# Kernel optimization log

Hardware: AMD Instinct MI355X
Metric: run time of the kernel (lower is better)

The kernel has to match this reference:

```python
import jax, jax.numpy as jnp
import numpy as np


def setup_inputs() -> dict:
    key = jax.random.key(0)
    k1, k2, k3, k4, k5 = jax.random.split(key, 5)
    B, S, E, H, D = 8, 1024, 1024, 8, 128  # batch, seq, embed, heads, hidden/head
    stdv = 1.0 / np.sqrt(D)
    return {
        "k": jax.random.normal(k1, (B, S, E), jnp.float32),
        "q": jax.random.normal(k2, (B, S, E), jnp.float32),
        "flag": 0,  # False: project q through w_qx
        "w_kx": jax.random.uniform(k3, (H, E, D), jnp.float32, -stdv, stdv),
        "w_qx": jax.random.uniform(k4, (H, E, D), jnp.float32, -stdv, stdv),
        "proj_w": jax.random.normal(k5, (E, H * D), jnp.float32) * 0.02,  # out_dim = embed_dim
        "proj_b": jnp.zeros((E,), jnp.float32),
    }


def reference(k, q, flag, w_kx, w_qx, proj_w, proj_b):
    H, E, D = w_kx.shape
    B, Sk, _ = k.shape
    Sq = q.shape[1]
    # per-head tanh projections: [H, B, S, D]
    kx = jnp.tanh(jnp.einsum("bse,hed->hbsd", k, w_kx))
    if flag:
        qx = jnp.broadcast_to(q[None], (H,) + q.shape)  # q already in hidden space
    else:
        qx = jnp.tanh(jnp.einsum("bse,hed->hbsd", q, w_qx))
    # scaled dot product scores [H, B, Sq, Sk]
    score = jnp.einsum("hbqd,hbkd->hbqk", qx, kx) / jnp.sqrt(jnp.float32(D))
    attn = jax.nn.softmax(score, axis=-1)
    out = jnp.einsum("hbqk,hbkd->hbqd", attn, kx)  # [H, B, Sq, D]
    # concat heads: [B, Sq, H*D], then output projection (dropout p=0 is identity)
    out = jnp.transpose(out, (1, 2, 0, 3)).reshape(B, Sq, H * D)
    return out @ proj_w.T + proj_b
```

## Files before the change

### kernel.cpp

```cpp
#include <hip/hip_runtime.h>

typedef unsigned short u16;
typedef unsigned int u32;
typedef __bf16 bf16x8 __attribute__((ext_vector_type(8)));
typedef float f32x4 __attribute__((ext_vector_type(4)));

#define MFMA16(a, b, c) __builtin_amdgcn_mfma_f32_16x16x32_bf16(a, b, c, 0, 0, 0)
#define EXP2(x) __builtin_amdgcn_exp2f(x)

typedef const void __attribute__((address_space(1)))* gas1_t;
typedef void __attribute__((address_space(3)))* las3_t;

__device__ __forceinline__ void gload16(const void* g, void* l) {
  __builtin_amdgcn_global_load_lds((gas1_t)g, (las3_t)l, 16, 0, 0);
}

__device__ __forceinline__ u16 f2bf(float f) {
  union { float f; u32 u; } v; v.f = f;
  u32 r = v.u + 0x7FFFu + ((v.u >> 16) & 1u);
  return (u16)(r >> 16);
}

__device__ __forceinline__ float fast_tanh(float x) {
  float xc = fminf(fmaxf(x, -20.f), 20.f);
  float t = EXP2(xc * 2.885390081777927f);
  return (t - 1.0f) * __builtin_amdgcn_rcpf(t + 1.0f);
}

__global__ __launch_bounds__(256) void cvt_kernel(const float* __restrict__ in,
                                                  u16* __restrict__ out, int n8) {
  int i = blockIdx.x * blockDim.x + threadIdx.x;
  int stride = gridDim.x * blockDim.x;
  for (; i < n8; i += stride) {
    const float4* p = (const float4*)(in + (size_t)i * 8);
    float4 a = p[0], b = p[1];
    u16 t[8];
    t[0] = f2bf(a.x); t[1] = f2bf(a.y); t[2] = f2bf(a.z); t[3] = f2bf(a.w);
    t[4] = f2bf(b.x); t[5] = f2bf(b.y); t[6] = f2bf(b.z); t[7] = f2bf(b.w);
    *(uint4*)(out + (size_t)i * 8) = *(uint4*)t;
  }
}

__global__ __launch_bounds__(256) void wtrans_kernel(const float* __restrict__ w,
                                                     u16* __restrict__ wT) {
  __shared__ float t[64][65];
  int h = blockIdx.z;
  int e0 = blockIdx.x * 64, d0 = blockIdx.y * 64;
  const float* src = w + (size_t)h * 1024 * 128;
  u16* dst = wT + (size_t)h * 128 * 1024;
  int tid = threadIdx.x;
  {
    int row = tid >> 2, c0 = (tid & 3) * 16;
#pragma unroll
    for (int i = 0; i < 4; ++i) {
      float4 v = *(const float4*)(src + (size_t)(e0 + row) * 128 + d0 + c0 + i * 4);
      t[row][c0 + i * 4 + 0] = v.x;
      t[row][c0 + i * 4 + 1] = v.y;
      t[row][c0 + i * 4 + 2] = v.z;
      t[row][c0 + i * 4 + 3] = v.w;
    }
  }
  __syncthreads();
  {
    int dl = tid >> 2, c0 = (tid & 3) * 16;
    u16 tmp[16];
#pragma unroll
    for (int i = 0; i < 16; ++i) tmp[i] = f2bf(t[c0 + i][dl]);
    u16* o = dst + (size_t)(d0 + dl) * 1024 + e0 + c0;
    *(uint4*)o = *(uint4*)tmp;
    *(uint4*)(o + 8) = *(uint4*)(tmp + 8);
  }
}


template <int BM>
__device__ __forceinline__ void gemm8_core(const u16* __restrict__ Ab,
                                           const u16* __restrict__ Bb,
                                           int K, u16* lds,
                                           f32x4 (&acc)[BM / 32][4]) {
  constexpr int MH = BM / 64;
  constexpr int HR = BM / 4;
  constexpr int AH = (BM / 2) * 64;
  constexpr int BH = 128 * 64;
  constexpr int BUF = 2 * AH + 2 * BH;
  constexpr int LA = BM / 128;
  const int tid = threadIdx.x, lane = tid & 63, wid = tid >> 6;
  const int wr = wid >> 2, wc = wid & 3, l15 = lane & 15, g = lane >> 4;
  const int nkt = K >> 6;
  const int arow = wr * HR;
  const int brow = wc * 32;

  auto stageA = [&](u16* dstHalf, int mh, int kt) {
#pragma unroll
    for (int i = 0; i < LA; ++i) {
      int c = (wid * LA + i) * 64 + lane;
      int rr = c >> 3, src = (c & 7) ^ (rr & 7);
      int grow = (rr / HR) * (2 * HR) + mh * HR + (rr % HR);
      gload16((const char*)Ab + ((size_t)grow * K + kt * 64 + src * 8) * 2,
              (char*)dstHalf + c * 16);
    }
  };
  auto stageB = [&](u16* dstHalf, int nh, int kt) {
#pragma unroll
    for (int i = 0; i < 2; ++i) {
      int c = (wid * 2 + i) * 64 + lane;
      int cc = c >> 3, src = (c & 7) ^ (cc & 7);
      int gcol = (cc >> 5) * 64 + nh * 32 + (cc & 31);
      gload16((const char*)Bb + ((size_t)gcol * K + kt * 64 + src * 8) * 2,
              (char*)dstHalf + c * 16);
    }
  };

#define LDAF(half)                                                              \
  _Pragma("unroll") for (int m = 0; m < MH; ++m)                                \
  _Pragma("unroll") for (int kc = 0; kc < 2; ++kc) {                            \
    int r_ = arow + m * 16 + l15;                                               \
    af[m][kc] = *(const bf16x8*)((half) + r_ * 64 + (((kc * 4 + g) ^ (r_ & 7)) << 3)); \
  }
#define LDBF(half)                                                              \
  _Pragma("unroll") for (int n = 0; n < 2; ++n)                                 \
  _Pragma("unroll") for (int kc = 0; kc < 2; ++kc) {                            \
    int r_ = brow + n * 16 + l15;                                               \
    bb[n][kc] = *(const bf16x8*)((half) + r_ * 64 + (((kc * 4 + g) ^ (r_ & 7)) << 3)); \
  }
#define MFMAQ(MB, NB)                                                           \
  __builtin_amdgcn_s_setprio(1);                                                \
  _Pragma("unroll") for (int m = 0; m < MH; ++m)                                \
  _Pragma("unroll") for (int n = 0; n < 2; ++n)                                 \
  _Pragma("unroll") for (int kc = 0; kc < 2; ++kc)                              \
    acc[(MB) * MH + m][(NB) * 2 + n] =                                          \
        MFMA16(af[m][kc], bb[n][kc], acc[(MB) * MH + m][(NB) * 2 + n]);         \
  __builtin_amdgcn_s_setprio(0);

  stageA(lds, 0, 0);
  stageB(lds + 2 * AH, 0, 0);
  stageA(lds + AH, 1, 0);
  stageB(lds + 2 * AH + BH, 1, 0);
  if constexpr (BM == 256) asm volatile("s_waitcnt vmcnt(4)" ::: "memory");
  else                     asm volatile("s_waitcnt vmcnt(3)" ::: "memory");
  __builtin_amdgcn_s_barrier();

  bf16x8 af[MH][2], bb[2][2];
  for (int t = 0; t < nkt; ++t) {
    const int cur = t & 1;
    u16* A0c = lds + cur * BUF;
    u16* A1c = A0c + AH;
    u16* B0c = A0c + 2 * AH;
    u16* B1c = B0c + BH;
    u16* A0n = lds + (cur ^ 1) * BUF;
    u16* A1n = A0n + AH;
    u16* B0n = A0n + 2 * AH;
    u16* B1n = B0n + BH;
    const bool pf = (t + 1 < nkt);
    const int k1 = t + 1;

    asm volatile("s_waitcnt vmcnt(2)" ::: "memory");
    LDAF(A0c);
    LDBF(B0c);
    if (pf) stageA(A0n, 0, k1);
    __builtin_amdgcn_s_barrier();
    MFMAQ(0, 0);
    __builtin_amdgcn_s_barrier();

    if (pf) {
      if constexpr (BM == 256) asm volatile("s_waitcnt vmcnt(2)" ::: "memory");
      else                     asm volatile("s_waitcnt vmcnt(1)" ::: "memory");
    } else {
      asm volatile("s_waitcnt vmcnt(0)" ::: "memory");
    }
    LDAF(A1c);
    if (pf) stageB(B0n, 0, k1);
    __builtin_amdgcn_s_barrier();
    MFMAQ(1, 0);
    __builtin_amdgcn_s_barrier();

    LDBF(B1c);
    if (pf) stageA(A1n, 1, k1);
    __builtin_amdgcn_s_barrier();
    MFMAQ(1, 1);
    __builtin_amdgcn_s_barrier();

    if (pf) {
      if constexpr (BM == 256) asm volatile("s_waitcnt vmcnt(2)" ::: "memory");
      else                     asm volatile("s_waitcnt vmcnt(1)" ::: "memory");
    }
    LDAF(A0c);
    if (pf) stageB(B1n, 1, k1);
    __builtin_amdgcn_s_barrier();
    MFMAQ(0, 1);
    __builtin_amdgcn_s_barrier();
  }
#undef LDAF
#undef LDBF
#undef MFMAQ
}

__global__ __launch_bounds__(512, 2) void gemm_tanh_kernel(
    const u16* __restrict__ Ak, const u16* __restrict__ Aq,
    const u16* __restrict__ wTk, const u16* __restrict__ wTq,
    u16* __restrict__ kxo, u16* __restrict__ qxo) {
  __shared__ alignas(16) u16 lds[2 * (2 * 128 * 64 + 2 * 128 * 64)];
  const u16* A; const u16* W; u16* C;
  if (blockIdx.z == 0) { A = Ak; W = wTk; C = kxo; }
  else { A = Aq; W = wTq; C = qxo; }
  int mBase = blockIdx.x * 256;
  int nBase = blockIdx.y * 256;
  f32x4 acc[8][4];
#pragma unroll
  for (int i = 0; i < 8; ++i)
#pragma unroll
    for (int j = 0; j < 4; ++j) acc[i][j] = (f32x4){0.f, 0.f, 0.f, 0.f};
  gemm8_core<256>(A + (size_t)mBase * 1024, W + (size_t)nBase * 1024, 1024,
                  lds, acc);
  const int lane = threadIdx.x & 63, wid = threadIdx.x >> 6;
  const int wr = wid >> 2, wc = wid & 3, l15 = lane & 15, g = lane >> 4;
#pragma unroll
  for (int mf = 0; mf < 8; ++mf)
#pragma unroll
    for (int nf = 0; nf < 4; ++nf)
#pragma unroll
      for (int j = 0; j < 4; ++j) {
        int m = mBase + wr * 128 + mf * 16 + g * 4 + j;
        int n = nBase + wc * 64 + nf * 16 + l15;
        int h = n >> 7, d = n & 127;
        C[(size_t)h * 8192 * 128 + (size_t)m * 128 + d] =
            f2bf(fast_tanh(acc[mf][nf][j]));
      }
}

__global__ __launch_bounds__(256) void transpose_kernel(const u16* __restrict__ kx,
                                                        u16* __restrict__ kxT) {
  __shared__ u16 t[64][72];
  int hb = blockIdx.z;
  const u16* src = kx + (size_t)hb * 1024 * 128;
  u16* dst = kxT + (size_t)hb * 128 * 1024;
  int s0 = blockIdx.x * 64, d0 = blockIdx.y * 64;
  int tid = threadIdx.x;
#pragma unroll
  for (int r = 0; r < 2; ++r) {
    int row = r * 32 + (tid >> 3), c8 = (tid & 7) * 8;
    uint4 v = *(const uint4*)(src + (size_t)(s0 + row) * 128 + d0 + c8);
    *(uint4*)&t[row][c8] = v;
  }
  __syncthreads();
#pragma unroll
  for (int r = 0; r < 2; ++r) {
    int dl = r * 32 + (tid >> 3), s8 = (tid & 7) * 8;
    u16 tmp[8];
#pragma unroll
    for (int i = 0; i < 8; ++i) tmp[i] = t[s8 + i][dl];
    *(uint4*)(dst + (size_t)(d0 + dl) * 1024 + s0 + s8) = *(uint4*)tmp;
  }
}

__global__ __launch_bounds__(256, 2) void attn_kernel(const u16* __restrict__ qx,
                                                      const u16* __restrict__ kx,
                                                      const u16* __restrict__ kxT,
                                                      u16* __restrict__ X) {
  __shared__ alignas(16) u16 Klds[2][64 * 128];
  __shared__ alignas(16) u16 Vlds[2][128 * 64];
  __shared__ alignas(16) u16 Plds[4][32 * 64];
  const int tid = threadIdx.x, lane = tid & 63, wid = tid >> 6;
  const int g = lane >> 4;
  const int hb = blockIdx.x, qt = blockIdx.y, h = hb >> 3, b = hb & 7;
  const u16* qxh = qx + ((size_t)h * 8192 + (size_t)b * 1024) * 128;
  const u16* kxh = kx + ((size_t)h * 8192 + (size_t)b * 1024) * 128;
  const u16* kxTh = kxT + (size_t)hb * 128 * 1024;
  const int q0 = qt * 128 + wid * 32;
  const float SC = 0.08838834764831845f * 1.44269504088896340f;

#define STAGE(buf, kt_)                                                        \
  do {                                                                         \
    _Pragma("unroll") for (int i_ = 0; i_ < 4; ++i_) {                         \
      int cIdx = (wid * 4 + i_) * 64 + lane;                                   \
      {                                                                        \
        int row = cIdx >> 4, slot = cIdx & 15;                                 \
        int src = slot ^ (row & 7);                                            \
        gload16((const char*)kxh + (size_t)((kt_) * 64 + row) * 256 + src * 16,\
                (char*)&Klds[buf][0] + (wid * 4 + i_) * 1024);                 \
      }                                                                        \
      {                                                                        \
        int row = cIdx >> 3, slot = cIdx & 7;                                  \
        int src = slot ^ (row & 7);                                            \
        gload16((const char*)kxTh + (size_t)row * 2048 + (kt_) * 128 + src * 16,\
                (char*)&Vlds[buf][0] + (wid * 4 + i_) * 1024);                 \
      }                                                                        \
    }                                                                          \
  } while (0)

  bf16x8 qa[2][4];
#pragma unroll
  for (int m = 0; m < 2; ++m)
#pragma unroll
    for (int kc = 0; kc < 4; ++kc)
      qa[m][kc] = *(const bf16x8*)(qxh + (size_t)(q0 + m * 16 + (lane & 15)) * 128
                                   + kc * 32 + g * 8);

  f32x4 os[2][8];
#pragma unroll
  for (int i = 0; i < 2; ++i)
#pragma unroll
    for (int j = 0; j < 8; ++j) os[i][j] = (f32x4){0.f, 0.f, 0.f, 0.f};
  float lsum[2] = {0.f, 0.f};

  u16* Pw = &Plds[wid][0];

  STAGE(0, 0);

  for (int kt = 0; kt < 16; ++kt) {
    const int cur = kt & 1;
    if (kt < 15) {
      STAGE(cur ^ 1, kt + 1);
      asm volatile("s_waitcnt vmcnt(8)" ::: "memory");
    } else {
      asm volatile("s_waitcnt vmcnt(0)" ::: "memory");
    }
    __builtin_amdgcn_s_barrier();

    const u16* Kc = &Klds[cur][0];
    const u16* Vc = &Vlds[cur][0];

    f32x4 sa[4][2];
#pragma unroll
    for (int i = 0; i < 4; ++i)
#pragma unroll
      for (int j = 0; j < 2; ++j) sa[i][j] = (f32x4){0.f, 0.f, 0.f, 0.f};
    __builtin_amdgcn_s_setprio(1);
#pragma unroll
    for (int kc = 0; kc < 4; ++kc) {
      bf16x8 kb[4];
#pragma unroll
      for (int t = 0; t < 4; ++t) {
        int row = t * 16 + (lane & 15);
        int ch = kc * 4 + g;
        kb[t] = *(const bf16x8*)(Kc + row * 128 + ((ch ^ (row & 7)) << 3));
      }
#pragma unroll
      for (int t = 0; t < 4; ++t)
#pragma unroll
        for (int m = 0; m < 2; ++m)
          sa[t][m] = MFMA16(kb[t], qa[m][kc], sa[t][m]);
    }
    __builtin_amdgcn_s_setprio(0);

#pragma unroll
    for (int m = 0; m < 2; ++m) {
      int q = m * 16 + (lane & 15);
      int rowb = q * 128, q7 = q & 7;
#pragma unroll
      for (int t = 0; t < 4; ++t) {
        float p0 = EXP2(sa[t][m][0] * SC);
        float p1 = EXP2(sa[t][m][1] * SC);
        float p2 = EXP2(sa[t][m][2] * SC);
        float p3 = EXP2(sa[t][m][3] * SC);
        lsum[m] += (p0 + p1) + (p2 + p3);
        uint2 pk;
        pk.x = (u32)f2bf(p0) | ((u32)f2bf(p1) << 16);
        pk.y = (u32)f2bf(p2) | ((u32)f2bf(p3) << 16);
        int slot = (2 * t + (g >> 1)) ^ q7;
        *(uint2*)((char*)Pw + rowb + slot * 16 + 8 * (g & 1)) = pk;
      }
    }

    __builtin_amdgcn_s_setprio(1);
#pragma unroll
    for (int kc2 = 0; kc2 < 2; ++kc2) {
      bf16x8 pa[2], vb[8];
#pragma unroll
      for (int m = 0; m < 2; ++m) {
        int q = m * 16 + (lane & 15);
        int slot = (g + 4 * kc2) ^ (q & 7);
        pa[m] = *(const bf16x8*)((char*)Pw + q * 128 + slot * 16);
      }
#pragma unroll
      for (int nd = 0; nd < 8; ++nd) {
        int row = nd * 16 + (lane & 15);
        int ch = kc2 * 4 + g;
        vb[nd] = *(const bf16x8*)(Vc + row * 64 + ((ch ^ (row & 7)) << 3));
      }
#pragma unroll
      for (int m = 0; m < 2; ++m)
#pragma unroll
        for (int nd = 0; nd < 8; ++nd)
          os[m][nd] = MFMA16(pa[m], vb[nd], os[m][nd]);
    }
    __builtin_amdgcn_s_setprio(0);
    __builtin_amdgcn_s_barrier();
  }
#undef STAGE

#pragma unroll
  for (int m = 0; m < 2; ++m) {
    float s = lsum[m];
    s += __shfl_xor(s, 16);
    s += __shfl_xor(s, 32);
    lsum[m] = s;
  }

#pragma unroll
  for (int m = 0; m < 2; ++m)
#pragma unroll
    for (int j = 0; j < 4; ++j) {
      float tot = __shfl(lsum[m], 4 * g + j, 64);
      float inv = 1.f / tot;
      int qrow = b * 1024 + q0 + m * 16 + g * 4 + j;
#pragma unroll
      for (int nd = 0; nd < 8; ++nd) {
        int col = h * 128 + nd * 16 + (lane & 15);
        X[(size_t)qrow * 1024 + col] = f2bf(os[m][nd][j] * inv);
      }
    }
}

__global__ __launch_bounds__(512, 2) void gemm_bias_kernel(
    const u16* __restrict__ X, const u16* __restrict__ pw,
    const float* __restrict__ pb, float* __restrict__ out) {
  __shared__ alignas(16) u16 lds[2 * (2 * 64 * 64 + 2 * 128 * 64)];
  int mBase = blockIdx.x * 128;
  int nBase = blockIdx.y * 256;
  f32x4 acc[4][4];
#pragma unroll
  for (int i = 0; i < 4; ++i)
#pragma unroll
    for (int j = 0; j < 4; ++j) acc[i][j] = (f32x4){0.f, 0.f, 0.f, 0.f};
  gemm8_core<128>(X + (size_t)mBase * 1024, pw + (size_t)nBase * 1024, 1024,
                  lds, acc);
  const int lane = threadIdx.x & 63, wid = threadIdx.x >> 6;
  const int wr = wid >> 2, wc = wid & 3, l15 = lane & 15, g = lane >> 4;
#pragma unroll
  for (int nf = 0; nf < 4; ++nf) {
    int e = nBase + wc * 64 + nf * 16 + l15;
    float bv = pb[e];
#pragma unroll
    for (int mf = 0; mf < 4; ++mf)
#pragma unroll
      for (int j = 0; j < 4; ++j) {
        int m = mBase + wr * 64 + mf * 16 + g * 4 + j;
        out[(size_t)m * 1024 + e] = acc[mf][nf][j] + bv;
      }
  }
}

extern "C" void kernel_launch(void* const* d_in, const int* in_sizes, int n_in,
                              void* d_out, int out_size, void* d_ws, size_t ws_size,
                              hipStream_t stream) {
  const float* k = (const float*)d_in[0];
  const float* q = (const float*)d_in[1];
  const float* wk = (const float*)d_in[3];
  const float* wq = (const float*)d_in[4];
  const float* pw = (const float*)d_in[5];
  const float* pb = (const float*)d_in[6];
  float* out = (float*)d_out;
  char* ws = (char*)d_ws;

  u16* kbf = (u16*)(ws);
  u16* qbf = (u16*)(ws + (16ull << 20));
  u16* wTk = (u16*)(ws + (32ull << 20));
  u16* wTq = (u16*)(ws + (34ull << 20));
  u16* pwb = (u16*)(ws + (36ull << 20));
  u16* kx  = (u16*)(ws + (38ull << 20));
  u16* qx  = (u16*)(ws + (54ull << 20));
  u16* kxT = (u16*)(ws + (70ull << 20));
  u16* X   = kbf;

  cvt_kernel<<<2048, 256, 0, stream>>>(k, kbf, 1048576);
  cvt_kernel<<<2048, 256, 0, stream>>>(q, qbf, 1048576);
  cvt_kernel<<<512, 256, 0, stream>>>(pw, pwb, 131072);
  wtrans_kernel<<<dim3(16, 2, 8), 256, 0, stream>>>(wk, wTk);
  wtrans_kernel<<<dim3(16, 2, 8), 256, 0, stream>>>(wq, wTq);
  gemm_tanh_kernel<<<dim3(32, 4, 2), 512, 0, stream>>>(kbf, qbf, wTk, wTq, kx, qx);
  transpose_kernel<<<dim3(16, 2, 64), 256, 0, stream>>>(kx, kxT);
  attn_kernel<<<dim3(64, 8), 256, 0, stream>>>(qx, kx, kxT, X);
  gemm_bias_kernel<<<dim3(64, 4), 512, 0, stream>>>(X, pwb, pb, out);
}
```

Before: 137.5 us.

## Fuse kx transpose into projection GEMM, widen attention blocks, reorder grid

The projection GEMM epilogue now also writes the transposed K tile, which removes the separate transpose kernel launch and its extra read and write of kx. The attention kernel now runs 512 threads per block, covering 256 queries per block with 8 waves, so each staged K/V tile is shared across more query rows. Each wave issues fewer loads per stage, and the wait count is adjusted to match. The grid axes for both GEMMs are swapped so consecutive blocks share the same A rows, and the LDS destination for the global-to-LDS loads is rewritten as a per-wave base. Risks are uncoalesced 8-byte strided stores for kxT in the epilogue and lower attention occupancy at the larger block size.

```diff
diff --git a/kernel.cpp b/kernel.cpp
--- a/kernel.cpp
+++ b/kernel.cpp
@@ -71,7 +71,6 @@
     *(uint4*)(o + 8) = *(uint4*)(tmp + 8);
   }
 }
-
 
 template <int BM>
 __device__ __forceinline__ void gemm8_core(const u16* __restrict__ Ab,
@@ -97,7 +96,7 @@
       int rr = c >> 3, src = (c & 7) ^ (rr & 7);
       int grow = (rr / HR) * (2 * HR) + mh * HR + (rr % HR);
       gload16((const char*)Ab + ((size_t)grow * K + kt * 64 + src * 8) * 2,
-              (char*)dstHalf + c * 16);
+              (char*)dstHalf + (wid * LA + i) * 1024);
     }
   };
   auto stageB = [&](u16* dstHalf, int nh, int kt) {
@@ -107,7 +106,7 @@
       int cc = c >> 3, src = (c & 7) ^ (cc & 7);
       int gcol = (cc >> 5) * 64 + nh * 32 + (cc & 31);
       gload16((const char*)Bb + ((size_t)gcol * K + kt * 64 + src * 8) * 2,
-              (char*)dstHalf + c * 16);
+              (char*)dstHalf + (wid * 2 + i) * 1024);
     }
   };
 
@@ -198,13 +197,14 @@
 __global__ __launch_bounds__(512, 2) void gemm_tanh_kernel(
     const u16* __restrict__ Ak, const u16* __restrict__ Aq,
     const u16* __restrict__ wTk, const u16* __restrict__ wTq,
-    u16* __restrict__ kxo, u16* __restrict__ qxo) {
+    u16* __restrict__ kxo, u16* __restrict__ qxo, u16* __restrict__ kxT) {
   __shared__ alignas(16) u16 lds[2 * (2 * 128 * 64 + 2 * 128 * 64)];
   const u16* A; const u16* W; u16* C;
   if (blockIdx.z == 0) { A = Ak; W = wTk; C = kxo; }
   else { A = Aq; W = wTq; C = qxo; }
-  int mBase = blockIdx.x * 256;
-  int nBase = blockIdx.y * 256;
+  const bool isK = (blockIdx.z == 0);
+  int nBase = blockIdx.x * 256;
+  int mBase = blockIdx.y * 256;
   f32x4 acc[8][4];
 #pragma unroll
   for (int i = 0; i < 8; ++i)
@@ -217,73 +217,55 @@
 #pragma unroll
   for (int mf = 0; mf < 8; ++mf)
 #pragma unroll
-    for (int nf = 0; nf < 4; ++nf)
+    for (int nf = 0; nf < 4; ++nf) {
+      int m0 = mBase + wr * 128 + mf * 16 + g * 4;
+      int n = nBase + wc * 64 + nf * 16 + l15;
+      int h = n >> 7, d = n & 127;
+      u16 t4[4];
 #pragma unroll
       for (int j = 0; j < 4; ++j) {
-        int m = mBase + wr * 128 + mf * 16 + g * 4 + j;
-        int n = nBase + wc * 64 + nf * 16 + l15;
-        int h = n >> 7, d = n & 127;
-        C[(size_t)h * 8192 * 128 + (size_t)m * 128 + d] =
-            f2bf(fast_tanh(acc[mf][nf][j]));
-      }
-}
-
-__global__ __launch_bounds__(256) void transpose_kernel(const u16* __restrict__ kx,
-                                                        u16* __restrict__ kxT) {
-  __shared__ u16 t[64][72];
-  int hb = blockIdx.z;
-  const u16* src = kx + (size_t)hb * 1024 * 128;
-  u16* dst = kxT + (size_t)hb * 128 * 1024;
-  int s0 = blockIdx.x * 64, d0 = blockIdx.y * 64;
-  int tid = threadIdx.x;
-#pragma unroll
-  for (int r = 0; r < 2; ++r) {
-    int row = r * 32 + (tid >> 3), c8 = (tid & 7) * 8;
-    uint4 v = *(const uint4*)(src + (size_t)(s0 + row) * 128 + d0 + c8);
-    *(uint4*)&t[row][c8] = v;
-  }
-  __syncthreads();
-#pragma unroll
-  for (int r = 0; r < 2; ++r) {
-    int dl = r * 32 + (tid >> 3), s8 = (tid & 7) * 8;
-    u16 tmp[8];
-#pragma unroll
-    for (int i = 0; i < 8; ++i) tmp[i] = t[s8 + i][dl];
-    *(uint4*)(dst + (size_t)(d0 + dl) * 1024 + s0 + s8) = *(uint4*)tmp;
-  }
-}
-
-__global__ __launch_bounds__(256, 2) void attn_kernel(const u16* __restrict__ qx,
+        t4[j] = f2bf(fast_tanh(acc[mf][nf][j]));
+        C[(size_t)h * 8192 * 128 + (size_t)(m0 + j) * 128 + d] = t4[j];
+      }
+      if (isK) {
+        int b = m0 >> 10, s0 = m0 & 1023;
+        *(uint2*)(kxT + (size_t)(h * 8 + b) * 131072 + (size_t)d * 1024 + s0) =
+            *(uint2*)t4;
+      }
+    }
+}
+
+__global__ __launch_bounds__(512, 2) void attn_kernel(const u16* __restrict__ qx,
                                                       const u16* __restrict__ kx,
                                                       const u16* __restrict__ kxT,
                                                       u16* __restrict__ X) {
   __shared__ alignas(16) u16 Klds[2][64 * 128];
   __shared__ alignas(16) u16 Vlds[2][128 * 64];
-  __shared__ alignas(16) u16 Plds[4][32 * 64];
+  __shared__ alignas(16) u16 Plds[8][32 * 64];
   const int tid = threadIdx.x, lane = tid & 63, wid = tid >> 6;
   const int g = lane >> 4;
   const int hb = blockIdx.x, qt = blockIdx.y, h = hb >> 3, b = hb & 7;
   const u16* qxh = qx + ((size_t)h * 8192 + (size_t)b * 1024) * 128;
   const u16* kxh = kx + ((size_t)h * 8192 + (size_t)b * 1024) * 128;
   const u16* kxTh = kxT + (size_t)hb * 128 * 1024;
-  const int q0 = qt * 128 + wid * 32;
+  const int q0 = qt * 256 + wid * 32;
   const float SC = 0.08838834764831845f * 1.44269504088896340f;
 
 #define STAGE(buf, kt_)                                                        \
   do {                                                                         \
-    _Pragma("unroll") for (int i_ = 0; i_ < 4; ++i_) {                         \
-      int cIdx = (wid * 4 + i_) * 64 + lane;                                   \
+    _Pragma("unroll") for (int i_ = 0; i_ < 2; ++i_) {                         \
+      int cIdx = (wid * 2 + i_) * 64 + lane;                                   \
       {                                                                        \
         int row = cIdx >> 4, slot = cIdx & 15;                                 \
         int src = slot ^ (row & 7);                                            \
         gload16((const char*)kxh + (size_t)((kt_) * 64 + row) * 256 + src * 16,\
-                (char*)&Klds[buf][0] + (wid * 4 + i_) * 1024);                 \
+                (char*)&Klds[buf][0] + (wid * 2 + i_) * 1024);                 \
       }                                                                        \
       {                                                                        \
         int row = cIdx >> 3, slot = cIdx & 7;                                  \
         int src = slot ^ (row & 7);                                            \
         gload16((const char*)kxTh + (size_t)row * 2048 + (kt_) * 128 + src * 16,\
-                (char*)&Vlds[buf][0] + (wid * 4 + i_) * 1024);                 \
+                (char*)&Vlds[buf][0] + (wid * 2 + i_) * 1024);                 \
       }                                                                        \
     }                                                                          \
   } while (0)
@@ -311,7 +293,7 @@
     const int cur = kt & 1;
     if (kt < 15) {
       STAGE(cur ^ 1, kt + 1);
-      asm volatile("s_waitcnt vmcnt(8)" ::: "memory");
+      asm volatile("s_waitcnt vmcnt(4)" ::: "memory");
     } else {
       asm volatile("s_waitcnt vmcnt(0)" ::: "memory");
     }
@@ -416,8 +398,8 @@
     const u16* __restrict__ X, const u16* __restrict__ pw,
     const float* __restrict__ pb, float* __restrict__ out) {
   __shared__ alignas(16) u16 lds[2 * (2 * 64 * 64 + 2 * 128 * 64)];
-  int mBase = blockIdx.x * 128;
-  int nBase = blockIdx.y * 256;
+  int nBase = blockIdx.x * 256;
+  int mBase = blockIdx.y * 128;
   f32x4 acc[4][4];
 #pragma unroll
   for (int i = 0; i < 4; ++i)
@@ -468,8 +450,8 @@
   cvt_kernel<<<512, 256, 0, stream>>>(pw, pwb, 131072);
   wtrans_kernel<<<dim3(16, 2, 8), 256, 0, stream>>>(wk, wTk);
   wtrans_kernel<<<dim3(16, 2, 8), 256, 0, stream>>>(wq, wTq);
-  gemm_tanh_kernel<<<dim3(32, 4, 2), 512, 0, stream>>>(kbf, qbf, wTk, wTq, kx, qx);
-  transpose_kernel<<<dim3(16, 2, 64), 256, 0, stream>>>(kx, kxT);
-  attn_kernel<<<dim3(64, 8), 256, 0, stream>>>(qx, kx, kxT, X);
-  gemm_bias_kernel<<<dim3(64, 4), 512, 0, stream>>>(X, pwb, pb, out);
-}
+  gemm_tanh_kernel<<<dim3(4, 32, 2), 512, 0, stream>>>(kbf, qbf, wTk, wTq,
+                                                       kx, qx, kxT);
+  attn_kernel<<<dim3(64, 4), 512, 0, stream>>>(qx, kx, kxT, X);
+  gemm_bias_kernel<<<dim3(4, 64), 512, 0, stream>>>(X, pwb, pb, out);
+}
```

Result: slower. 141.7 us (+3.0%).
